# Optimization experiments

Hardware: AMD Instinct MI355X
Metric: run time of the kernel (lower is better)

## Reference

```python
import jax, jax.numpy as jnp
import numpy as np

N_NODES = 100000
N_EDGES = 1600000
D_IN = 128
D_OUT = 128

def setup_inputs() -> dict:
    key = jax.random.key(0)
    k1, k2, k3, k4, k5 = jax.random.split(key, 5)
    h = jax.random.normal(k1, (N_NODES, D_IN), dtype=jnp.float32)
    src = jax.random.randint(k2, (N_EDGES,), 0, N_NODES, dtype=jnp.int64)
    dst = jax.random.randint(k3, (N_EDGES,), 0, N_NODES, dtype=jnp.int64)
    # Xavier-ish init for the two linear maps (fc_self, fc_neigh), no bias
    scale = 1.0 / np.sqrt(D_IN)
    W_self = jax.random.normal(k4, (D_IN, D_OUT), dtype=jnp.float32) * scale
    W_neigh = jax.random.normal(k5, (D_IN, D_OUT), dtype=jnp.float32) * scale
    return {"h": h, "src": src, "dst": dst, "W_self": W_self, "W_neigh": W_neigh}

def reference(h, src, dst, W_self, W_neigh):
    # DGL SAGEConv mean aggregator, bias=False:
    #   h_neigh[v] = mean_{(u->v) in E} h[u]   (0 if v has no in-edges)
    #   out = h @ W_self + h_neigh @ W_neigh
    msg = h[src]  # [E, D_IN] neighbor gather
    neigh_sum = jax.ops.segment_sum(msg, dst, num_segments=N_NODES)  # [N, D_IN]
    deg = jax.ops.segment_sum(jnp.ones((src.shape[0],), dtype=h.dtype), dst,
                              num_segments=N_NODES)  # [N]
    h_neigh = neigh_sum / jnp.maximum(deg, 1.0)[:, None]
    return h @ W_self + h_neigh @ W_neigh
```

## Files before the change

### kernel.cpp

```cpp
#include <hip/hip_runtime.h>


constexpr int NN = 100000;
constexpr int NE = 1600000;
constexpr int D  = 128;
constexpr int BK = 64;
constexpr int NB = (NN + BK - 1) / BK;
constexpr int PB = 8192;
constexpr int CAPB = 1536;
constexpr int XST = 258;
constexpr int PADI = 32;
constexpr int PART_BLOCKS = (NE + PB - 1) / PB;
constexpr int WPK_BLOCKS  = 16;
constexpr int CVT_BLOCKS  = NN * D / 8 / 256;

typedef __attribute__((ext_vector_type(8))) short short8;
typedef __attribute__((ext_vector_type(4))) float floatx4;
typedef __attribute__((ext_vector_type(2))) float floatx2;

static __device__ __forceinline__ unsigned short f2bf(float f) {
    unsigned u = __float_as_uint(f);
    unsigned r = ((u >> 16) & 1u) + 0x7fffu;
    return (unsigned short)((u + r) >> 16);
}

__global__ __launch_bounds__(256) void k_prep(
    const float* __restrict__ h, const float* __restrict__ Wself,
    const float* __restrict__ Wneigh, const int* __restrict__ src,
    const int* __restrict__ dst, uint2* __restrict__ hf8,
    unsigned short* __restrict__ Wp, int* __restrict__ bcursor,
    unsigned* __restrict__ packed)
{
    const int t = threadIdx.x;
    if (blockIdx.x < PART_BLOCKS) {
        __shared__ int lh[NB];
        const int e0 = blockIdx.x * PB;
        for (int i = t; i < NB; i += 256) lh[i] = 0;
        __syncthreads();

        int myd[32], msrc[32];
#pragma unroll
        for (int j = 0; j < 32; ++j) {
            int e = e0 + j * 256 + t;
            myd[j] = (e < NE) ? dst[e] : -1;
        }
#pragma unroll
        for (int j = 0; j < 32; ++j) {
            int e = e0 + j * 256 + t;
            msrc[j] = (e < NE) ? src[e] : 0;
        }
#pragma unroll
        for (int j = 0; j < 32; ++j)
            if (myd[j] >= 0) atomicAdd(&lh[myd[j] >> 6], 1);
        __syncthreads();
        for (int i = t; i < NB; i += 256) {
            int c = lh[i];
            if (c) lh[i] = atomicAdd(&bcursor[(size_t)i * PADI], c);
        }
        __syncthreads();
#pragma unroll
        for (int j = 0; j < 32; ++j) {
            if (myd[j] >= 0) {
                int b = myd[j] >> 6;
                int pos = atomicAdd(&lh[b], 1);
                if (pos < CAPB)
                    packed[(size_t)b * CAPB + pos] =
                        (unsigned)msrc[j] | ((unsigned)(myd[j] & 63) << 17);
            }
        }
    } else if (blockIdx.x < PART_BLOCKS + WPK_BLOCKS) {
        int kg  = (blockIdx.x - PART_BLOCKS) * 2 + (t >> 7);
        int col = t & 127;
        unsigned short v[8];
#pragma unroll
        for (int j = 0; j < 8; ++j) {
            int k = kg * 8 + j;
            const float* W = (k < 128) ? (Wself + (size_t)k * D)
                                       : (Wneigh + (size_t)(k - 128) * D);
            v[j] = f2bf(W[col]);
        }
        uint4 o;
        o.x = (unsigned)v[0] | ((unsigned)v[1] << 16);
        o.y = (unsigned)v[2] | ((unsigned)v[3] << 16);
        o.z = (unsigned)v[4] | ((unsigned)v[5] << 16);
        o.w = (unsigned)v[6] | ((unsigned)v[7] << 16);
        ((uint4*)Wp)[kg * 128 + col] = o;
    } else {
        int i = (blockIdx.x - PART_BLOCKS - WPK_BLOCKS) * 256 + t;
        const float4* h4 = (const float4*)h;
        float4 a = h4[(size_t)i * 2];
        float4 b = h4[(size_t)i * 2 + 1];
        unsigned q0 = __builtin_amdgcn_cvt_pk_fp8_f32(a.x, a.y, 0u, false);
        q0          = __builtin_amdgcn_cvt_pk_fp8_f32(a.z, a.w, q0, true);
        unsigned q1 = __builtin_amdgcn_cvt_pk_fp8_f32(b.x, b.y, 0u, false);
        q1          = __builtin_amdgcn_cvt_pk_fp8_f32(b.z, b.w, q1, true);
        hf8[i] = make_uint2(q0, q1);
    }
}

__global__ __launch_bounds__(512) void k_agg_gemm(
    const float* __restrict__ h, const uint2* __restrict__ hf8,
    const int* __restrict__ bcursor, const unsigned* __restrict__ packed,
    const unsigned short* __restrict__ Wp, float* __restrict__ out)
{
    __shared__ unsigned short Xs[BK][XST];
    __shared__ unsigned sorted[CAPB];
    __shared__ int cnt[BK], offs[BK], cur[BK];

    const int t      = threadIdx.x;
    const int bucket = blockIdx.x;
    const size_t ebeg = (size_t)bucket * CAPB;
    const int ecnt   = min(bcursor[(size_t)bucket * PADI], CAPB);

    if (t < BK) cnt[t] = 0;

    {
        int row = t >> 3, seg = t & 7;
        int grow = min(bucket * BK + row, NN - 1);
        const float4* hp = (const float4*)(h + (size_t)grow * D + seg * 16);
        float4 f0 = hp[0], f1 = hp[1], f2 = hp[2], f3 = hp[3];
        uint4 q0, q1;
        q0.x = (unsigned)f2bf(f0.x) | ((unsigned)f2bf(f0.y) << 16);
        q0.y = (unsigned)f2bf(f0.z) | ((unsigned)f2bf(f0.w) << 16);
        q0.z = (unsigned)f2bf(f1.x) | ((unsigned)f2bf(f1.y) << 16);
        q0.w = (unsigned)f2bf(f1.z) | ((unsigned)f2bf(f1.w) << 16);
        q1.x = (unsigned)f2bf(f2.x) | ((unsigned)f2bf(f2.y) << 16);
        q1.y = (unsigned)f2bf(f2.z) | ((unsigned)f2bf(f2.w) << 16);
        q1.z = (unsigned)f2bf(f3.x) | ((unsigned)f2bf(f3.y) << 16);
        q1.w = (unsigned)f2bf(f3.z) | ((unsigned)f2bf(f3.w) << 16);
        *(uint4*)&Xs[row][seg * 16]     = q0;
        *(uint4*)&Xs[row][seg * 16 + 8] = q1;
    }
    __syncthreads();

    unsigned pk[3];
#pragma unroll
    for (int i = 0; i < 3; ++i) {
        int idx = t + i * 512;
        pk[i] = (idx < ecnt) ? packed[ebeg + idx] : 0u;
    }
#pragma unroll
    for (int i = 0; i < 3; ++i) {
        int idx = t + i * 512;
        if (idx < ecnt) atomicAdd(&cnt[(pk[i] >> 17) & 63u], 1);
    }
    __syncthreads();
    if (t < BK) {
        int v = cnt[t];
        int sum = v;
#pragma unroll
        for (int off = 1; off < 64; off <<= 1) {
            int u = __shfl_up(sum, off, 64);
            if (t >= off) sum += u;
        }
        offs[t] = sum - v;
        cur[t]  = sum - v;
    }
    __syncthreads();
#pragma unroll
    for (int i = 0; i < 3; ++i) {
        int idx = t + i * 512;
        if (idx < ecnt) {
            int pos = atomicAdd(&cur[(pk[i] >> 17) & 63u], 1);
            sorted[pos] = pk[i] & 0x1FFFFu;
        }
    }
    __syncthreads();

    {
        const int g  = t >> 3;
        const int l8 = t & 7;
        const int beg = offs[g];
        const int n   = cnt[g];
        const uint4* __restrict__ hr = (const uint4*)hf8;

        floatx2 ac[8];
#pragma unroll
        for (int j = 0; j < 8; ++j) ac[j] = (floatx2){0.f, 0.f};

#define ACC16(X) do {                                                         \
            unsigned ww0 = (X).x, ww1 = (X).y, ww2 = (X).z, ww3 = (X).w;      \
            ac[0] += __builtin_amdgcn_cvt_pk_f32_fp8(ww0, false);             \
            ac[1] += __builtin_amdgcn_cvt_pk_f32_fp8(ww0, true);              \
            ac[2] += __builtin_amdgcn_cvt_pk_f32_fp8(ww1, false);             \
            ac[3] += __builtin_amdgcn_cvt_pk_f32_fp8(ww1, true);              \
            ac[4] += __builtin_amdgcn_cvt_pk_f32_fp8(ww2, false);             \
            ac[5] += __builtin_amdgcn_cvt_pk_f32_fp8(ww2, true);              \
            ac[6] += __builtin_amdgcn_cvt_pk_f32_fp8(ww3, false);             \
            ac[7] += __builtin_amdgcn_cvt_pk_f32_fp8(ww3, true);              \
        } while (0)

        int e = 0;
        for (; e + 3 < n; e += 4) {
            uint4 x0 = hr[(size_t)sorted[beg + e]     * 8 + l8];
            uint4 x1 = hr[(size_t)sorted[beg + e + 1] * 8 + l8];
            uint4 x2 = hr[(size_t)sorted[beg + e + 2] * 8 + l8];
            uint4 x3 = hr[(size_t)sorted[beg + e + 3] * 8 + l8];
            ACC16(x0); ACC16(x1); ACC16(x2); ACC16(x3);
        }
        for (; e + 1 < n; e += 2) {
            uint4 x0 = hr[(size_t)sorted[beg + e]     * 8 + l8];
            uint4 x1 = hr[(size_t)sorted[beg + e + 1] * 8 + l8];
            ACC16(x0); ACC16(x1);
        }
        if (e < n) {
            uint4 x0 = hr[(size_t)sorted[beg + e] * 8 + l8];
            ACC16(x0);
        }
#undef ACC16

        float inv = (n > 0) ? 1.0f / (float)n : 0.0f;
        unsigned short m[16];
#pragma unroll
        for (int j = 0; j < 8; ++j) {
            m[j * 2]     = f2bf(ac[j].x * inv);
            m[j * 2 + 1] = f2bf(ac[j].y * inv);
        }
        uint4 o0, o1;
        o0.x = (unsigned)m[0]  | ((unsigned)m[1]  << 16);
        o0.y = (unsigned)m[2]  | ((unsigned)m[3]  << 16);
        o0.z = (unsigned)m[4]  | ((unsigned)m[5]  << 16);
        o0.w = (unsigned)m[6]  | ((unsigned)m[7]  << 16);
        o1.x = (unsigned)m[8]  | ((unsigned)m[9]  << 16);
        o1.y = (unsigned)m[10] | ((unsigned)m[11] << 16);
        o1.z = (unsigned)m[12] | ((unsigned)m[13] << 16);
        o1.w = (unsigned)m[14] | ((unsigned)m[15] << 16);
        *(uint4*)&Xs[g][128 + l8 * 16]     = o0;
        *(uint4*)&Xs[g][128 + l8 * 16 + 8] = o1;
    }
    __syncthreads();

    const int wave  = t >> 6;
    const int lane  = t & 63;
    const int wl16  = lane & 15;
    const int kg4   = lane >> 4;
    const int wrow  = wave & 3;
    const int chalf = wave >> 2;
    floatx4 acc[4];
#pragma unroll
    for (int c = 0; c < 4; ++c) acc[c] = (floatx4){0.f, 0.f, 0.f, 0.f};

    const int arow = wrow * 16 + wl16;
#pragma unroll
    for (int ks = 0; ks < 8; ++ks) {
        const short8 a = *(const short8*)&Xs[arow][ks * 32 + kg4 * 8];
#pragma unroll
        for (int c = 0; c < 4; ++c) {
            const int ct = chalf * 4 + c;
            const short8 b = *(const short8*)(Wp + (((ks * 4 + kg4) * 128) + ct * 16 + wl16) * 8);
            acc[c] = __builtin_amdgcn_mfma_f32_16x16x32_bf16(a, b, acc[c], 0, 0, 0);
        }
    }

    const int rbase = bucket * BK + wrow * 16 + kg4 * 4;
#pragma unroll
    for (int r = 0; r < 4; ++r) {
        int row = rbase + r;
        if (row < NN) {
            float* o = out + (size_t)row * D + chalf * 64 + wl16;
#pragma unroll
            for (int c = 0; c < 4; ++c)
                o[c * 16] = acc[c][r];
        }
    }
}

extern "C" void kernel_launch(void* const* d_in, const int* in_sizes, int n_in,
                              void* d_out, int out_size, void* d_ws, size_t ws_size,
                              hipStream_t stream) {
    const float* h      = (const float*)d_in[0];
    const int*   src    = (const int*)d_in[1];
    const int*   dst    = (const int*)d_in[2];
    const float* Wself  = (const float*)d_in[3];
    const float* Wneigh = (const float*)d_in[4];
    float*       out    = (float*)d_out;

    uint2* hf8         = (uint2*)d_ws;
    unsigned short* Wp = (unsigned short*)(hf8 + (size_t)NN * D / 8);
    unsigned* packed   = (unsigned*)(Wp + 256 * D);
    uintptr_t bc_a     = ((uintptr_t)(packed + (size_t)NB * CAPB) + 255) & ~(uintptr_t)255;
    int* bcursor       = (int*)bc_a;

    hipMemsetAsync(bcursor, 0, (size_t)NB * PADI * sizeof(int), stream);

    k_prep     <<<dim3(PART_BLOCKS + WPK_BLOCKS + CVT_BLOCKS), 256, 0, stream>>>(
                   h, Wself, Wneigh, src, dst, hf8, Wp, bcursor, packed);
    k_agg_gemm <<<dim3(NB), 512, 0, stream>>>(h, hf8, bcursor, packed, Wp, out);
}
```

Before: 185.1 us.

## Replace single-pass edge bucketing with two-level radix partition via superbuckets

Edge partitioning now runs in two levels. First, edges are scattered into 49 superbuckets of 2048 nodes, sorted locally in shared memory so the global writes are contiguous. A new kernel then splits each superbucket into 32 buckets of 64 nodes. This targets the scattered per-edge writes and the heavy global atomic contention of the old single pass over roughly 1563 buckets, at the cost of an extra kernel launch and an extra round trip of the edge list through memory. The gather loop in the aggregation kernel is also unrolled from 4 to 6 loads to raise memory-level parallelism.

```diff
diff --git a/kernel.cpp b/kernel.cpp
--- a/kernel.cpp
+++ b/kernel.cpp
@@ -6,8 +6,11 @@
 constexpr int D  = 128;
 constexpr int BK = 64;
 constexpr int NB = (NN + BK - 1) / BK;
+constexpr int NS = (NN + 2047) / 2048;
 constexpr int PB = 8192;
 constexpr int CAPB = 1536;
+constexpr int CAPS = 40960;
+constexpr int CHUNKS = CAPS / PB;
 constexpr int XST = 258;
 constexpr int PADI = 32;
 constexpr int PART_BLOCKS = (NE + PB - 1) / PB;
@@ -28,14 +31,17 @@
     const float* __restrict__ h, const float* __restrict__ Wself,
     const float* __restrict__ Wneigh, const int* __restrict__ src,
     const int* __restrict__ dst, uint2* __restrict__ hf8,
-    unsigned short* __restrict__ Wp, int* __restrict__ bcursor,
-    unsigned* __restrict__ packed)
+    unsigned short* __restrict__ Wp, int* __restrict__ scnt,
+    unsigned* __restrict__ packed1)
 {
     const int t = threadIdx.x;
     if (blockIdx.x < PART_BLOCKS) {
-        __shared__ int lh[NB];
+        __shared__ unsigned srt[PB];
+        __shared__ int sh[NS], sbeg[NS], scur[NS], sgb[NS];
         const int e0 = blockIdx.x * PB;
-        for (int i = t; i < NB; i += 256) lh[i] = 0;
+        const int total = min(PB, NE - e0);
+
+        for (int i = t; i < NS; i += 256) sh[i] = 0;
         __syncthreads();
 
         int myd[32], msrc[32];
@@ -51,21 +57,44 @@
         }
 #pragma unroll
         for (int j = 0; j < 32; ++j)
-            if (myd[j] >= 0) atomicAdd(&lh[myd[j] >> 6], 1);
+            if (myd[j] >= 0) atomicAdd(&sh[myd[j] >> 11], 1);
         __syncthreads();
-        for (int i = t; i < NB; i += 256) {
-            int c = lh[i];
-            if (c) lh[i] = atomicAdd(&bcursor[(size_t)i * PADI], c);
+        if (t < 64) {
+            int v = (t < NS) ? sh[t] : 0;
+            int sum = v;
+#pragma unroll
+            for (int off = 1; off < 64; off <<= 1) {
+                int u = __shfl_up(sum, off, 64);
+                if (t >= off) sum += u;
+            }
+            if (t < NS) {
+                sbeg[t] = sum - v;
+                scur[t] = sum - v;
+                sgb[t]  = v ? atomicAdd(&scnt[(size_t)t * PADI], v) : 0;
+            }
         }
         __syncthreads();
 #pragma unroll
         for (int j = 0; j < 32; ++j) {
             if (myd[j] >= 0) {
-                int b = myd[j] >> 6;
-                int pos = atomicAdd(&lh[b], 1);
-                if (pos < CAPB)
-                    packed[(size_t)b * CAPB + pos] =
-                        (unsigned)msrc[j] | ((unsigned)(myd[j] & 63) << 17);
+                int s = myd[j] >> 11;
+                int p = atomicAdd(&scur[s], 1);
+                srt[p] = (unsigned)msrc[j] | ((unsigned)(myd[j] & 2047) << 17);
+            }
+        }
+        __syncthreads();
+#pragma unroll
+        for (int j = 0; j < 32; ++j) {
+            int i = t + j * 256;
+            if (i < total) {
+                int lo = 0, hi = NS - 1;
+                while (lo < hi) {
+                    int mid = (lo + hi + 1) >> 1;
+                    if (sbeg[mid] <= i) lo = mid; else hi = mid - 1;
+                }
+                int gp = sgb[lo] + (i - sbeg[lo]);
+                if (gp < CAPS)
+                    packed1[(size_t)lo * CAPS + gp] = srt[i];
             }
         }
     } else if (blockIdx.x < PART_BLOCKS + WPK_BLOCKS) {
@@ -98,6 +127,72 @@
     }
 }
 
+__global__ __launch_bounds__(256) void k_part2(
+    const unsigned* __restrict__ packed1, const int* __restrict__ scnt,
+    int* __restrict__ bcursor, unsigned* __restrict__ packed2)
+{
+    const int t  = threadIdx.x;
+    const int sb = blockIdx.x / CHUNKS;
+    const int ck = blockIdx.x % CHUNKS;
+    const int sc = min(scnt[(size_t)sb * PADI], CAPS);
+    const int beg = ck * PB;
+    const int m  = min(PB, sc - beg);
+    if (m <= 0) return;
+
+    __shared__ unsigned srt[PB];
+    __shared__ int fh[32], fbeg[32], fcur[32], fgb[32];
+
+    if (t < 32) fh[t] = 0;
+    __syncthreads();
+
+    unsigned v[32];
+#pragma unroll
+    for (int j = 0; j < 32; ++j) {
+        int idx = t + j * 256;
+        v[j] = (idx < m) ? packed1[(size_t)sb * CAPS + beg + idx] : 0xFFFFFFFFu;
+    }
+#pragma unroll
+    for (int j = 0; j < 32; ++j) {
+        int idx = t + j * 256;
+        if (idx < m) atomicAdd(&fh[(v[j] >> 23) & 31u], 1);
+    }
+    __syncthreads();
+    if (t < 32) {
+        int c = fh[t];
+        int sum = c;
+#pragma unroll
+        for (int off = 1; off < 32; off <<= 1) {
+            int u = __shfl_up(sum, off, 64);
+            if (t >= off) sum += u;
+        }
+        fbeg[t] = sum - c;
+        fcur[t] = sum - c;
+        int b = sb * 32 + t;
+        fgb[t] = (c && b < NB) ? atomicAdd(&bcursor[(size_t)b * PADI], c) : 0;
+    }
+    __syncthreads();
+#pragma unroll
+    for (int j = 0; j < 32; ++j) {
+        int idx = t + j * 256;
+        if (idx < m) {
+            int p = atomicAdd(&fcur[(v[j] >> 23) & 31u], 1);
+            srt[p] = v[j];
+        }
+    }
+    __syncthreads();
+#pragma unroll
+    for (int j = 0; j < 32; ++j) {
+        int i = t + j * 256;
+        if (i < m) {
+            unsigned w = srt[i];
+            int f  = (w >> 23) & 31u;
+            int gp = fgb[f] + (i - fbeg[f]);
+            if (gp < CAPB)
+                packed2[(size_t)(sb * 32 + f) * CAPB + gp] = w & 0x7FFFFFu;
+        }
+    }
+}
+
 __global__ __launch_bounds__(512) void k_agg_gemm(
     const float* __restrict__ h, const uint2* __restrict__ hf8,
     const int* __restrict__ bcursor, const unsigned* __restrict__ packed,
@@ -191,12 +286,15 @@
         } while (0)
 
         int e = 0;
-        for (; e + 3 < n; e += 4) {
+        for (; e + 5 < n; e += 6) {
             uint4 x0 = hr[(size_t)sorted[beg + e]     * 8 + l8];
             uint4 x1 = hr[(size_t)sorted[beg + e + 1] * 8 + l8];
             uint4 x2 = hr[(size_t)sorted[beg + e + 2] * 8 + l8];
             uint4 x3 = hr[(size_t)sorted[beg + e + 3] * 8 + l8];
-            ACC16(x0); ACC16(x1); ACC16(x2); ACC16(x3);
+            uint4 x4 = hr[(size_t)sorted[beg + e + 4] * 8 + l8];
+            uint4 x5 = hr[(size_t)sorted[beg + e + 5] * 8 + l8];
+            ACC16(x0); ACC16(x1); ACC16(x2);
+            ACC16(x3); ACC16(x4); ACC16(x5);
         }
         for (; e + 1 < n; e += 2) {
             uint4 x0 = hr[(size_t)sorted[beg + e]     * 8 + l8];
@@ -277,13 +375,16 @@
 
     uint2* hf8         = (uint2*)d_ws;
     unsigned short* Wp = (unsigned short*)(hf8 + (size_t)NN * D / 8);
-    unsigned* packed   = (unsigned*)(Wp + 256 * D);
-    uintptr_t bc_a     = ((uintptr_t)(packed + (size_t)NB * CAPB) + 255) & ~(uintptr_t)255;
+    unsigned* packed2  = (unsigned*)(Wp + 256 * D);
+    unsigned* packed1  = packed2 + (size_t)NB * CAPB;
+    uintptr_t bc_a     = ((uintptr_t)(packed1 + (size_t)NS * CAPS) + 255) & ~(uintptr_t)255;
     int* bcursor       = (int*)bc_a;
-
-    hipMemsetAsync(bcursor, 0, (size_t)NB * PADI * sizeof(int), stream);
+    int* scnt          = bcursor + (size_t)NB * PADI;
+
+    hipMemsetAsync(bcursor, 0, (size_t)(NB + NS) * PADI * sizeof(int), stream);
 
     k_prep     <<<dim3(PART_BLOCKS + WPK_BLOCKS + CVT_BLOCKS), 256, 0, stream>>>(
-                   h, Wself, Wneigh, src, dst, hf8, Wp, bcursor, packed);
-    k_agg_gemm <<<dim3(NB), 512, 0, stream>>>(h, hf8, bcursor, packed, Wp, out);
-}
+                   h, Wself, Wneigh, src, dst, hf8, Wp, scnt, packed1);
+    k_part2    <<<dim3(NS * CHUNKS), 256, 0, stream>>>(packed1, scnt, bcursor, packed2);
+    k_agg_gemm <<<dim3(NB), 512, 0, stream>>>(h, hf8, bcursor, packed2, Wp, out);
+}
```

Result: no change. 186.1 us (+0.6%).

## Fuse prep and aggregate-GEMM into one cooperative persistent kernel with grid sync

Applied to the files above, without the earlier changes.

Merges the partition/weight-pack/fp8-convert prep kernel and the gather-aggregate-GEMM kernel into a single cooperative kernel. A grid-wide sync separates the two phases, and a persistent grid strides over buckets. This removes one kernel launch boundary and the tail gap between the kernels, at the cost of grid-sync overhead and fewer resident blocks for the aggregation phase. It also widens the gather unroll from 4 to 6 edges and keeps a two-kernel fallback path.

```diff
diff --git a/kernel.cpp b/kernel.cpp
--- a/kernel.cpp
+++ b/kernel.cpp
@@ -1,4 +1,7 @@
 #include <hip/hip_runtime.h>
+#include <hip/hip_cooperative_groups.h>
+
+namespace cg = cooperative_groups;
 
 
 constexpr int NN = 100000;
@@ -11,8 +14,9 @@
 constexpr int XST = 258;
 constexpr int PADI = 32;
 constexpr int PART_BLOCKS = (NE + PB - 1) / PB;
-constexpr int WPK_BLOCKS  = 16;
-constexpr int CVT_BLOCKS  = NN * D / 8 / 256;
+constexpr int WPK_BLOCKS  = 8;
+constexpr int CVT_BASE    = PART_BLOCKS + WPK_BLOCKS;
+constexpr int NCVT_ITEMS  = NN * D / 8;
 
 typedef __attribute__((ext_vector_type(8))) short short8;
 typedef __attribute__((ext_vector_type(4))) float floatx4;
@@ -24,70 +28,79 @@
     return (unsigned short)((u + r) >> 16);
 }
 
-__global__ __launch_bounds__(256) void k_prep(
-    const float* __restrict__ h, const float* __restrict__ Wself,
-    const float* __restrict__ Wneigh, const int* __restrict__ src,
-    const int* __restrict__ dst, uint2* __restrict__ hf8,
-    unsigned short* __restrict__ Wp, int* __restrict__ bcursor,
-    unsigned* __restrict__ packed)
-{
-    const int t = threadIdx.x;
-    if (blockIdx.x < PART_BLOCKS) {
-        __shared__ int lh[NB];
-        const int e0 = blockIdx.x * PB;
-        for (int i = t; i < NB; i += 256) lh[i] = 0;
-        __syncthreads();
-
-        int myd[32], msrc[32];
-#pragma unroll
-        for (int j = 0; j < 32; ++j) {
-            int e = e0 + j * 256 + t;
-            myd[j] = (e < NE) ? dst[e] : -1;
-        }
-#pragma unroll
-        for (int j = 0; j < 32; ++j) {
-            int e = e0 + j * 256 + t;
-            msrc[j] = (e < NE) ? src[e] : 0;
-        }
-#pragma unroll
-        for (int j = 0; j < 32; ++j)
-            if (myd[j] >= 0) atomicAdd(&lh[myd[j] >> 6], 1);
-        __syncthreads();
-        for (int i = t; i < NB; i += 256) {
-            int c = lh[i];
-            if (c) lh[i] = atomicAdd(&bcursor[(size_t)i * PADI], c);
-        }
-        __syncthreads();
-#pragma unroll
-        for (int j = 0; j < 32; ++j) {
-            if (myd[j] >= 0) {
-                int b = myd[j] >> 6;
-                int pos = atomicAdd(&lh[b], 1);
-                if (pos < CAPB)
-                    packed[(size_t)b * CAPB + pos] =
-                        (unsigned)msrc[j] | ((unsigned)(myd[j] & 63) << 17);
-            }
-        }
-    } else if (blockIdx.x < PART_BLOCKS + WPK_BLOCKS) {
-        int kg  = (blockIdx.x - PART_BLOCKS) * 2 + (t >> 7);
-        int col = t & 127;
-        unsigned short v[8];
-#pragma unroll
-        for (int j = 0; j < 8; ++j) {
-            int k = kg * 8 + j;
-            const float* W = (k < 128) ? (Wself + (size_t)k * D)
-                                       : (Wneigh + (size_t)(k - 128) * D);
-            v[j] = f2bf(W[col]);
-        }
-        uint4 o;
-        o.x = (unsigned)v[0] | ((unsigned)v[1] << 16);
-        o.y = (unsigned)v[2] | ((unsigned)v[3] << 16);
-        o.z = (unsigned)v[4] | ((unsigned)v[5] << 16);
-        o.w = (unsigned)v[6] | ((unsigned)v[7] << 16);
-        ((uint4*)Wp)[kg * 128 + col] = o;
-    } else {
-        int i = (blockIdx.x - PART_BLOCKS - WPK_BLOCKS) * 256 + t;
-        const float4* h4 = (const float4*)h;
+struct SharedBlk {
+    unsigned short Xs[BK][XST];
+    unsigned sorted[CAPB];
+    int cnt[BK], offs[BK], cur[BK];
+};
+
+static __device__ __forceinline__ void do_part(
+    int t, int pb, const int* __restrict__ src, const int* __restrict__ dst,
+    int* __restrict__ bcursor, unsigned* __restrict__ packed, int* lh)
+{
+    const int e0 = pb * PB;
+    for (int i = t; i < NB; i += 512) lh[i] = 0;
+    __syncthreads();
+
+    int myd[16], msrc[16];
+#pragma unroll
+    for (int j = 0; j < 16; ++j) {
+        int e = e0 + j * 512 + t;
+        myd[j] = (e < NE) ? dst[e] : -1;
+    }
+#pragma unroll
+    for (int j = 0; j < 16; ++j) {
+        int e = e0 + j * 512 + t;
+        msrc[j] = (e < NE) ? src[e] : 0;
+    }
+#pragma unroll
+    for (int j = 0; j < 16; ++j)
+        if (myd[j] >= 0) atomicAdd(&lh[myd[j] >> 6], 1);
+    __syncthreads();
+    for (int i = t; i < NB; i += 512) {
+        int c = lh[i];
+        if (c) lh[i] = atomicAdd(&bcursor[(size_t)i * PADI], c);
+    }
+    __syncthreads();
+#pragma unroll
+    for (int j = 0; j < 16; ++j) {
+        if (myd[j] >= 0) {
+            int b = myd[j] >> 6;
+            int pos = atomicAdd(&lh[b], 1);
+            if (pos < CAPB)
+                packed[(size_t)b * CAPB + pos] =
+                    (unsigned)msrc[j] | ((unsigned)(myd[j] & 63) << 17);
+        }
+    }
+}
+
+static __device__ __forceinline__ void do_wpack(
+    int t, int wb, const float* __restrict__ Wself,
+    const float* __restrict__ Wneigh, unsigned short* __restrict__ Wp)
+{
+    int kg  = wb * 4 + (t >> 7);
+    int col = t & 127;
+    unsigned short v[8];
+#pragma unroll
+    for (int j = 0; j < 8; ++j) {
+        int k = kg * 8 + j;
+        const float* W = (k < 128) ? (Wself + (size_t)k * D)
+                                   : (Wneigh + (size_t)(k - 128) * D);
+        v[j] = f2bf(W[col]);
+    }
+    uint4 o;
+    o.x = (unsigned)v[0] | ((unsigned)v[1] << 16);
+    o.y = (unsigned)v[2] | ((unsigned)v[3] << 16);
+    o.z = (unsigned)v[4] | ((unsigned)v[5] << 16);
+    o.w = (unsigned)v[6] | ((unsigned)v[7] << 16);
+    ((uint4*)Wp)[kg * 128 + col] = o;
+}
+
+static __device__ __forceinline__ void do_cvt(
+    int idx0, int stride, const float* __restrict__ h, uint2* __restrict__ hf8)
+{
+    const float4* h4 = (const float4*)h;
+    for (int i = idx0; i < NCVT_ITEMS; i += stride) {
         float4 a = h4[(size_t)i * 2];
         float4 b = h4[(size_t)i * 2 + 1];
         unsigned q0 = __builtin_amdgcn_cvt_pk_fp8_f32(a.x, a.y, 0u, false);
@@ -98,21 +111,34 @@
     }
 }
 
-__global__ __launch_bounds__(512) void k_agg_gemm(
-    const float* __restrict__ h, const uint2* __restrict__ hf8,
-    const int* __restrict__ bcursor, const unsigned* __restrict__ packed,
-    const unsigned short* __restrict__ Wp, float* __restrict__ out)
-{
-    __shared__ unsigned short Xs[BK][XST];
-    __shared__ unsigned sorted[CAPB];
-    __shared__ int cnt[BK], offs[BK], cur[BK];
-
-    const int t      = threadIdx.x;
-    const int bucket = blockIdx.x;
+static __device__ __forceinline__ void phase1(
+    int t, int b, int G,
+    const float* __restrict__ h, const float* __restrict__ Wself,
+    const float* __restrict__ Wneigh, const int* __restrict__ src,
+    const int* __restrict__ dst, uint2* __restrict__ hf8,
+    unsigned short* __restrict__ Wp, int* __restrict__ bcursor,
+    unsigned* __restrict__ packed, int* lh)
+{
+    if (b < PART_BLOCKS) {
+        do_part(t, b, src, dst, bcursor, packed, lh);
+    } else if (b < CVT_BASE) {
+        do_wpack(t, b - PART_BLOCKS, Wself, Wneigh, Wp);
+    } else {
+        int nblk = G - CVT_BASE;
+        do_cvt((b - CVT_BASE) * 512 + t, nblk * 512, h, hf8);
+    }
+}
+
+static __device__ __forceinline__ void do_agg(
+    int t, int bucket, const float* __restrict__ h,
+    const uint2* __restrict__ hf8, const int* __restrict__ bcursor,
+    const unsigned* __restrict__ packed, const unsigned short* __restrict__ Wp,
+    float* __restrict__ out, SharedBlk& S)
+{
     const size_t ebeg = (size_t)bucket * CAPB;
     const int ecnt   = min(bcursor[(size_t)bucket * PADI], CAPB);
 
-    if (t < BK) cnt[t] = 0;
+    if (t < BK) S.cnt[t] = 0;
 
     {
         int row = t >> 3, seg = t & 7;
@@ -128,8 +154,8 @@
         q1.y = (unsigned)f2bf(f2.z) | ((unsigned)f2bf(f2.w) << 16);
         q1.z = (unsigned)f2bf(f3.x) | ((unsigned)f2bf(f3.y) << 16);
         q1.w = (unsigned)f2bf(f3.z) | ((unsigned)f2bf(f3.w) << 16);
-        *(uint4*)&Xs[row][seg * 16]     = q0;
-        *(uint4*)&Xs[row][seg * 16 + 8] = q1;
+        *(uint4*)&S.Xs[row][seg * 16]     = q0;
+        *(uint4*)&S.Xs[row][seg * 16 + 8] = q1;
     }
     __syncthreads();
 
@@ -142,27 +168,27 @@
 #pragma unroll
     for (int i = 0; i < 3; ++i) {
         int idx = t + i * 512;
-        if (idx < ecnt) atomicAdd(&cnt[(pk[i] >> 17) & 63u], 1);
+        if (idx < ecnt) atomicAdd(&S.cnt[(pk[i] >> 17) & 63u], 1);
     }
     __syncthreads();
     if (t < BK) {
-        int v = cnt[t];
+        int v = S.cnt[t];
         int sum = v;
 #pragma unroll
         for (int off = 1; off < 64; off <<= 1) {
             int u = __shfl_up(sum, off, 64);
             if (t >= off) sum += u;
         }
-        offs[t] = sum - v;
-        cur[t]  = sum - v;
+        S.offs[t] = sum - v;
+        S.cur[t]  = sum - v;
     }
     __syncthreads();
 #pragma unroll
     for (int i = 0; i < 3; ++i) {
         int idx = t + i * 512;
         if (idx < ecnt) {
-            int pos = atomicAdd(&cur[(pk[i] >> 17) & 63u], 1);
-            sorted[pos] = pk[i] & 0x1FFFFu;
+            int pos = atomicAdd(&S.cur[(pk[i] >> 17) & 63u], 1);
+            S.sorted[pos] = pk[i] & 0x1FFFFu;
         }
     }
     __syncthreads();
@@ -170,8 +196,8 @@
     {
         const int g  = t >> 3;
         const int l8 = t & 7;
-        const int beg = offs[g];
-        const int n   = cnt[g];
+        const int beg = S.offs[g];
+        const int n   = S.cnt[g];
         const uint4* __restrict__ hr = (const uint4*)hf8;
 
         floatx2 ac[8];
@@ -191,20 +217,23 @@
         } while (0)
 
         int e = 0;
-        for (; e + 3 < n; e += 4) {
-            uint4 x0 = hr[(size_t)sorted[beg + e]     * 8 + l8];
-            uint4 x1 = hr[(size_t)sorted[beg + e + 1] * 8 + l8];
-            uint4 x2 = hr[(size_t)sorted[beg + e + 2] * 8 + l8];
-            uint4 x3 = hr[(size_t)sorted[beg + e + 3] * 8 + l8];
-            ACC16(x0); ACC16(x1); ACC16(x2); ACC16(x3);
+        for (; e + 5 < n; e += 6) {
+            uint4 x0 = hr[(size_t)S.sorted[beg + e]     * 8 + l8];
+            uint4 x1 = hr[(size_t)S.sorted[beg + e + 1] * 8 + l8];
+            uint4 x2 = hr[(size_t)S.sorted[beg + e + 2] * 8 + l8];
+            uint4 x3 = hr[(size_t)S.sorted[beg + e + 3] * 8 + l8];
+            uint4 x4 = hr[(size_t)S.sorted[beg + e + 4] * 8 + l8];
+            uint4 x5 = hr[(size_t)S.sorted[beg + e + 5] * 8 + l8];
+            ACC16(x0); ACC16(x1); ACC16(x2);
+            ACC16(x3); ACC16(x4); ACC16(x5);
         }
         for (; e + 1 < n; e += 2) {
-            uint4 x0 = hr[(size_t)sorted[beg + e]     * 8 + l8];
-            uint4 x1 = hr[(size_t)sorted[beg + e + 1] * 8 + l8];
+            uint4 x0 = hr[(size_t)S.sorted[beg + e]     * 8 + l8];
+            uint4 x1 = hr[(size_t)S.sorted[beg + e + 1] * 8 + l8];
             ACC16(x0); ACC16(x1);
         }
         if (e < n) {
-            uint4 x0 = hr[(size_t)sorted[beg + e] * 8 + l8];
+            uint4 x0 = hr[(size_t)S.sorted[beg + e] * 8 + l8];
             ACC16(x0);
         }
 #undef ACC16
@@ -225,8 +254,8 @@
         o1.y = (unsigned)m[10] | ((unsigned)m[11] << 16);
         o1.z = (unsigned)m[12] | ((unsigned)m[13] << 16);
         o1.w = (unsigned)m[14] | ((unsigned)m[15] << 16);
-        *(uint4*)&Xs[g][128 + l8 * 16]     = o0;
-        *(uint4*)&Xs[g][128 + l8 * 16 + 8] = o1;
+        *(uint4*)&S.Xs[g][128 + l8 * 16]     = o0;
+        *(uint4*)&S.Xs[g][128 + l8 * 16 + 8] = o1;
     }
     __syncthreads();
 
@@ -243,7 +272,7 @@
     const int arow = wrow * 16 + wl16;
 #pragma unroll
     for (int ks = 0; ks < 8; ++ks) {
-        const short8 a = *(const short8*)&Xs[arow][ks * 32 + kg4 * 8];
+        const short8 a = *(const short8*)&S.Xs[arow][ks * 32 + kg4 * 8];
 #pragma unroll
         for (int c = 0; c < 4; ++c) {
             const int ct = chalf * 4 + c;
@@ -263,6 +292,52 @@
                 o[c * 16] = acc[c][r];
         }
     }
+}
+
+__global__ __launch_bounds__(512) void mega(
+    const float* __restrict__ h, const float* __restrict__ Wself,
+    const float* __restrict__ Wneigh, const int* __restrict__ src,
+    const int* __restrict__ dst, uint2* __restrict__ hf8,
+    unsigned short* __restrict__ Wp, int* __restrict__ bcursor,
+    unsigned* __restrict__ packed, float* __restrict__ out)
+{
+    __shared__ SharedBlk S;
+    const int t = threadIdx.x;
+    const int b = blockIdx.x;
+    const int G = gridDim.x;
+
+    phase1(t, b, G, h, Wself, Wneigh, src, dst, hf8, Wp, bcursor, packed,
+           (int*)&S);
+    __threadfence();
+    cg::this_grid().sync();
+
+    for (int bucket = b; bucket < NB; bucket += G) {
+        do_agg(t, bucket, h, hf8, bcursor, packed, Wp, out, S);
+        __syncthreads();
+    }
+}
+
+constexpr int FB_PREP_G = CVT_BASE + 800;
+
+__global__ __launch_bounds__(512) void k_prep_fb(
+    const float* __restrict__ h, const float* __restrict__ Wself,
+    const float* __restrict__ Wneigh, const int* __restrict__ src,
+    const int* __restrict__ dst, uint2* __restrict__ hf8,
+    unsigned short* __restrict__ Wp, int* __restrict__ bcursor,
+    unsigned* __restrict__ packed)
+{
+    __shared__ SharedBlk S;
+    phase1(threadIdx.x, blockIdx.x, (int)gridDim.x, h, Wself, Wneigh, src, dst,
+           hf8, Wp, bcursor, packed, (int*)&S);
+}
+
+__global__ __launch_bounds__(512) void k_agg_fb(
+    const float* __restrict__ h, const uint2* __restrict__ hf8,
+    const int* __restrict__ bcursor, const unsigned* __restrict__ packed,
+    const unsigned short* __restrict__ Wp, float* __restrict__ out)
+{
+    __shared__ SharedBlk S;
+    do_agg(threadIdx.x, blockIdx.x, h, hf8, bcursor, packed, Wp, out, S);
 }
 
 extern "C" void kernel_launch(void* const* d_in, const int* in_sizes, int n_in,
@@ -283,7 +358,21 @@
 
     hipMemsetAsync(bcursor, 0, (size_t)NB * PADI * sizeof(int), stream);
 
-    k_prep     <<<dim3(PART_BLOCKS + WPK_BLOCKS + CVT_BLOCKS), 256, 0, stream>>>(
-                   h, Wself, Wneigh, src, dst, hf8, Wp, bcursor, packed);
-    k_agg_gemm <<<dim3(NB), 512, 0, stream>>>(h, hf8, bcursor, packed, Wp, out);
-}
+    int mablk = 0;
+    hipError_t oe = hipOccupancyMaxActiveBlocksPerMultiprocessor(&mablk, mega, 512, 0);
+    int G = (oe == hipSuccess && mablk >= 1) ? mablk * 256 : 0;
+    if (G > 1024) G = 1024;
+
+    hipError_t le = hipErrorUnknown;
+    if (G >= 256) {
+        void* args[] = {(void*)&h, (void*)&Wself, (void*)&Wneigh, (void*)&src,
+                        (void*)&dst, (void*)&hf8, (void*)&Wp, (void*)&bcursor,
+                        (void*)&packed, (void*)&out};
+        le = hipLaunchCooperativeKernel(mega, dim3(G), dim3(512), args, 0u, stream);
+    }
+    if (le != hipSuccess) {
+        k_prep_fb<<<dim3(FB_PREP_G), 512, 0, stream>>>(
+            h, Wself, Wneigh, src, dst, hf8, Wp, bcursor, packed);
+        k_agg_fb <<<dim3(NB), 512, 0, stream>>>(h, hf8, bcursor, packed, Wp, out);
+    }
+}
```

Result: no change. 183.0 us (-1.2%).
